# Kernel tuning notes

Hardware: AMD Instinct MI355X
Metric: run time of the kernel (lower is better)

Reference implementation:

```python
import jax, jax.numpy as jnp
import numpy as np

N, E, D_FEAT, D_HID, N_CLASS, N_LAYER = 100000, 1600000, 128, 128, 40, 2


def _sage_layer(x, x_, src, dst, wl, wr, b, n):
    # mean aggregation of neighbor (src) features into dst nodes
    agg = jax.ops.segment_sum(x[src], dst, num_segments=n)          # [N, d_in]
    cnt = jax.ops.segment_sum(jnp.ones((src.shape[0], 1), x.dtype), dst, num_segments=n)
    agg = agg / jnp.maximum(cnt, 1.0)
    h = agg @ wl + x @ wr + b        # neighbor path + root path
    h_ = x_ @ wr + b                 # twin (detached-root) stream: root weight only
    return jax.nn.relu(h), jax.nn.relu(h_)


def setup_inputs() -> dict:
    key = jax.random.key(0)
    ks = jax.random.split(key, 12)
    s = 1.0 / np.sqrt(D_HID)
    inp = {
        "x": jax.random.normal(ks[0], (N, D_FEAT), jnp.float32),
        "edge_index1": jax.random.randint(ks[1], (2, E), 0, N, jnp.int32),
        "edge_index2": jax.random.randint(ks[2], (2, E), 0, N, jnp.int32),
        "wl1": jax.random.uniform(ks[3], (D_FEAT, D_HID), jnp.float32, -s, s),
        "wr1": jax.random.uniform(ks[4], (D_FEAT, D_HID), jnp.float32, -s, s),
        "b1": jnp.zeros((D_HID,), jnp.float32),
        "wl2": jax.random.uniform(ks[5], (D_HID, D_HID), jnp.float32, -s, s),
        "wr2": jax.random.uniform(ks[6], (D_HID, D_HID), jnp.float32, -s, s),
        "b2": jnp.zeros((D_HID,), jnp.float32),
        "w_out": jax.random.uniform(ks[7], (D_HID * N_LAYER, N_CLASS), jnp.float32, -s, s),
        "b_out": jnp.zeros((N_CLASS,), jnp.float32),
        "batch_size": N,
    }
    return inp


def reference(x, edge_index1, edge_index2, wl1, wr1, b1, wl2, wr2, b2, w_out, b_out, batch_size):
    n = x.shape[0]
    x_ = jax.lax.stop_gradient(x)[:batch_size]   # detached twin stream of root nodes
    # layer 1 (dropout is eval-mode no-op)
    h1, h1_ = _sage_layer(x, x_, edge_index1[0], edge_index1[1], wl1, wr1, b1, n)
    # layer 2
    h2, h2_ = _sage_layer(h1, h1_, edge_index2[0], edge_index2[1], wl2, wr2, b2, n)
    # jumping knowledge: mode 'cat' over per-layer root representations
    h = jnp.concatenate([h1[:batch_size], h2[:batch_size]], axis=-1)
    return h @ w_out + b_out
```

## Files before the change

kernel.cpp:

```cpp
#include <hip/hip_runtime.h>


#define MAXB  512
#define CAP   24
#define CAPS  6144
#define PBLK  384

typedef __attribute__((ext_vector_type(8))) short short8;
typedef __attribute__((ext_vector_type(4))) float floatx4;

__device__ __forceinline__ unsigned short f2b(float f) {
    unsigned u = __float_as_uint(f);
    unsigned r = (u + 0x7fffu + ((u >> 16) & 1u)) >> 16;
    return (unsigned short)r;
}
__device__ __forceinline__ float lo2f(unsigned u) { return __uint_as_float(u << 16); }
__device__ __forceinline__ float hi2f(unsigned u) { return __uint_as_float(u & 0xffff0000u); }
__device__ __forceinline__ unsigned pack2(float a, float b) {
    return (unsigned)f2b(a) | ((unsigned)f2b(b) << 16);
}

__global__ __launch_bounds__(256)
void prep_hist(const float4* __restrict__ x4, uint4* __restrict__ xb4, long n8,
               const float* __restrict__ wl1, const float* __restrict__ wr1,
               const float* __restrict__ wl2, const float* __restrict__ wr2,
               const float* __restrict__ wo,
               unsigned short* __restrict__ wt1, unsigned short* __restrict__ wt2,
               unsigned short* __restrict__ wot,
               const int* __restrict__ dst1, const int* __restrict__ dst2,
               int* __restrict__ hist1, int* __restrict__ hist2,
               int* __restrict__ bptr1, int* __restrict__ bptr2,
               int* __restrict__ done, int E, int nb) {
    long i = (long)blockIdx.x * 256 + threadIdx.x;
    if (i < n8) {
        float4 a = x4[i * 2];
        float4 b = x4[i * 2 + 1];
        uint4 o;
        o.x = pack2(a.x, a.y); o.y = pack2(a.z, a.w);
        o.z = pack2(b.x, b.y); o.w = pack2(b.z, b.w);
        xb4[i] = o;
    }
    if (i < 65536) {
        int l = (int)(i >> 15);
        int k5 = (int)(i & 32767);
        int j = k5 & 7, lane = (k5 >> 3) & 63, kb = (k5 >> 9) & 7, c = k5 >> 12;
        int k = kb * 32 + (lane >> 4) * 8 + j;
        int n = c * 16 + (lane & 15);
        const float* Wl = l ? wl2 : wl1;
        const float* Wr = l ? wr2 : wr1;
        float v = (k < 128) ? Wl[k * 128 + n] : Wr[(k - 128) * 128 + n];
        (l ? wt2 : wt1)[k5] = f2b(v);
    } else if (i < 65536 + 12288) {
        int k5 = (int)(i - 65536);
        int j = k5 & 7, lane = (k5 >> 3) & 63, kb = (k5 >> 9) & 7, c = k5 >> 12;
        int k = kb * 32 + (lane >> 4) * 8 + j;
        int col = c * 16 + (lane & 15);
        float v = (col < 40) ? wo[k * 40 + col] : 0.0f;
        wot[k5] = f2b(v);
    }
    __shared__ int h[MAXB];
    __shared__ int sticket;
    if (blockIdx.x < 512) {
        const int layer = blockIdx.x >> 8;
        const int bx    = blockIdx.x & 255;
        const int* dst  = layer ? dst2 : dst1;
        int* hist       = layer ? hist2 : hist1;
        for (int k = threadIdx.x; k < nb; k += 256) h[k] = 0;
        __syncthreads();
        for (int e = bx * 256 + threadIdx.x; e < E; e += 256 * 256)
            atomicAdd(&h[dst[e] >> 8], 1);
        __syncthreads();
        for (int k = threadIdx.x; k < nb; k += 256)
            if (h[k]) atomicAdd(&hist[k], h[k]);
        __threadfence();
        if (threadIdx.x == 0) sticket = atomicAdd(done, 1);
        __syncthreads();
        if (sticket == 511) {
            int* pair = h;
            const int tt = threadIdx.x;
            for (int l = 0; l < 2; ++l) {
                int* hist = l ? hist2 : hist1;
                int* bptr = l ? bptr2 : bptr1;
                int v0 = (2 * tt < nb)     ? atomicAdd(&hist[2 * tt], 0)     : 0;
                int v1 = (2 * tt + 1 < nb) ? atomicAdd(&hist[2 * tt + 1], 0) : 0;
                pair[tt] = v0 + v1;
                __syncthreads();
                for (int off = 1; off < 256; off <<= 1) {
                    int y = (tt >= off) ? pair[tt - off] : 0;
                    __syncthreads();
                    pair[tt] += y;
                    __syncthreads();
                }
                int ebase = pair[tt] - (v0 + v1);
                if (2 * tt < nb)     bptr[2 * tt]     = ebase;
                if (2 * tt + 1 < nb) bptr[2 * tt + 1] = ebase + v0;
                if (tt == 0) bptr[nb] = E;
                __syncthreads();
            }
        }
    }
}

struct PartSmem { unsigned stage[MAXB][CAP]; int lcnt[MAXB]; int sbase[MAXB]; };
struct SortSmem { int recs[CAPS]; int sorted[CAPS]; int hcnt[256]; int hoff[256]; };
struct FusedSmem { uint4 lds[16 * 16]; };

__device__ __forceinline__ void partition_body(const int* __restrict__ src,
        const int* __restrict__ dst, const int* __restrict__ bptr,
        int* __restrict__ gcur, int* __restrict__ part, int E, int nb,
        int chunk, int nchunks, PartSmem& s) {
    const int t = threadIdx.x;
    for (int i = t; i < nb; i += 256) s.lcnt[i] = 0;
    __syncthreads();
    const int per = (E + nchunks - 1) / nchunks;
    const int e0 = chunk * per;
    const int e1 = min(e0 + per, E);
    for (int e = e0 + t; e < e1; e += 256) {
        int d = dst[e];
        int b = d >> 8;
        unsigned rec = (unsigned)src[e] | ((unsigned)(d & 255) << 17);
        int p = atomicAdd(&s.lcnt[b], 1);
        if (p < CAP) s.stage[b][p] = rec;
        else {
            int g = atomicAdd(&gcur[b], 1);
            part[bptr[b] + g] = (int)rec;
        }
    }
    __syncthreads();
    for (int b = t; b < nb; b += 256) {
        int c = s.lcnt[b]; if (c > CAP) c = CAP;
        if (c > 0) s.sbase[b] = bptr[b] + atomicAdd(&gcur[b], c);
    }
    __syncthreads();
    const int wv = t >> 6, ln = t & 63;
    for (int b = wv; b < nb; b += 4) {
        int c = s.lcnt[b]; if (c > CAP) c = CAP;
        if (ln < c) part[s.sbase[b] + ln] = (int)s.stage[b][ln];
    }
}

__device__ __forceinline__ void sort_body(const int* __restrict__ bptr,
        const int* __restrict__ part, int* __restrict__ col,
        int* __restrict__ row_ptr, int b, int nb_total, int N, int E,
        SortSmem& s) {
    const int t = threadIdx.x;
    const int beg = bptr[b], end = bptr[b + 1];
    int cnt = end - beg;
    if (cnt > CAPS) cnt = CAPS;

    for (int i = t; i < cnt; i += 256) s.recs[i] = part[beg + i];
    s.hcnt[t] = 0;
    __syncthreads();
    for (int i = t; i < cnt; i += 256)
        atomicAdd(&s.hcnt[((unsigned)s.recs[i]) >> 17], 1);
    __syncthreads();

    int v = s.hcnt[t];
    s.hoff[t] = v;
    __syncthreads();
    for (int off = 1; off < 256; off <<= 1) {
        int y = (t >= off) ? s.hoff[t - off] : 0;
        __syncthreads();
        s.hoff[t] += y;
        __syncthreads();
    }
    int myoff = s.hoff[t] - v;

    int row = b * 256 + t;
    if (row <= N) row_ptr[row] = beg + myoff;
    if (b == nb_total - 1 && t == 0) row_ptr[N] = E;
    __syncthreads();
    s.hoff[t] = myoff;
    s.hcnt[t] = 0;
    __syncthreads();

    for (int i = t; i < cnt; i += 256) {
        unsigned rec = (unsigned)s.recs[i];
        int node = rec >> 17;
        int p = s.hoff[node] + atomicAdd(&s.hcnt[node], 1);
        s.sorted[p] = (int)(rec & 0x1FFFF);
    }
    __syncthreads();
    for (int i = t; i < cnt; i += 256) col[beg + i] = s.sorted[i];
}

__device__ __forceinline__ void gather_node(const uint4* __restrict__ xb,
                                            const int* __restrict__ col,
                                            int beg, int end, int lane,
                                            float acc[8]) {
    int e = beg;
    if (e + 8 <= end) {
        int cidx[8];
#pragma unroll
        for (int q = 0; q < 8; ++q) cidx[q] = col[e + q];
        for (;;) {
            uint4 v[8];
#pragma unroll
            for (int q = 0; q < 8; ++q) v[q] = xb[(size_t)cidx[q] * 16 + lane];
            e += 8;
            const bool more = (e + 8 <= end);
            if (more) {
#pragma unroll
                for (int q = 0; q < 8; ++q) cidx[q] = col[e + q];
            }
#pragma unroll
            for (int q = 0; q < 8; ++q) {
                acc[0] += lo2f(v[q].x); acc[1] += hi2f(v[q].x);
                acc[2] += lo2f(v[q].y); acc[3] += hi2f(v[q].y);
                acc[4] += lo2f(v[q].z); acc[5] += hi2f(v[q].z);
                acc[6] += lo2f(v[q].w); acc[7] += hi2f(v[q].w);
            }
            if (!more) break;
        }
    }
    for (; e + 3 < end; e += 4) {
        uint4 v[4];
#pragma unroll
        for (int q = 0; q < 4; ++q) v[q] = xb[(size_t)col[e + q] * 16 + lane];
#pragma unroll
        for (int q = 0; q < 4; ++q) {
            acc[0] += lo2f(v[q].x); acc[1] += hi2f(v[q].x);
            acc[2] += lo2f(v[q].y); acc[3] += hi2f(v[q].y);
            acc[4] += lo2f(v[q].z); acc[5] += hi2f(v[q].z);
            acc[6] += lo2f(v[q].w); acc[7] += hi2f(v[q].w);
        }
    }
    for (; e < end; ++e) {
        uint4 v0 = xb[(size_t)col[e] * 16 + lane];
        acc[0] += lo2f(v0.x); acc[1] += hi2f(v0.x);
        acc[2] += lo2f(v0.y); acc[3] += hi2f(v0.y);
        acc[4] += lo2f(v0.z); acc[5] += hi2f(v0.z);
        acc[6] += lo2f(v0.w); acc[7] += hi2f(v0.w);
    }
    float inv = 1.0f / fmaxf((float)(end - beg), 1.0f);
#pragma unroll
    for (int j = 0; j < 8; ++j) acc[j] *= inv;
}

#define LDS_SLOT(row, col4) ((row) * 16 + ((col4) ^ ((row) & 7)))

__device__ __forceinline__ void fused1_body(const uint4* __restrict__ xb,
        const int* __restrict__ row_ptr, const int* __restrict__ col,
        const unsigned short* __restrict__ Wt, const float* __restrict__ bias,
        unsigned short* __restrict__ Hb, int N, int tile, FusedSmem& s) {
    const int t = threadIdx.x;
    {
        const int lrow = t >> 4;
        const int lane = t & 15;
        const int node = tile * 16 + lrow;
        float acc[8];
#pragma unroll
        for (int j = 0; j < 8; ++j) acc[j] = 0.0f;
        if (node < N)
            gather_node(xb, col, row_ptr[node], row_ptr[node + 1], lane, acc);
        uint4 o;
        o.x = pack2(acc[0], acc[1]); o.y = pack2(acc[2], acc[3]);
        o.z = pack2(acc[4], acc[5]); o.w = pack2(acc[6], acc[7]);
        s.lds[LDS_SLOT(lrow, lane)] = o;
    }
    __syncthreads();

    const int wave = t >> 6;
    const int lane = t & 63;
    const int quad = lane >> 4;
    const int l16  = lane & 15;
    const int rowbase = tile * 16;

    floatx4 acc2[2] = {(floatx4){0.f,0.f,0.f,0.f}, (floatx4){0.f,0.f,0.f,0.f}};
    int arow = rowbase + l16; if (arow >= N) arow = N - 1;
    const unsigned short* Xs = (const unsigned short*)xb;
    const size_t aoff = (size_t)arow * 128 + quad * 8;

#pragma unroll
    for (int kb = 0; kb < 8; ++kb) {
        short8 a;
        if (kb < 4)
            a = __builtin_bit_cast(short8, s.lds[LDS_SLOT(l16, quad + (kb & 3) * 4)]);
        else
            a = __builtin_bit_cast(short8, *(const uint4*)(Xs + aoff + (kb & 3) * 32));
#pragma unroll
        for (int cc = 0; cc < 2; ++cc) {
            const int c = wave * 2 + cc;
            short8 b = __builtin_bit_cast(short8,
                *(const uint4*)(Wt + (size_t)(((c * 8 + kb) * 64 + lane) * 8)));
            acc2[cc] = __builtin_amdgcn_mfma_f32_16x16x32_bf16(a, b, acc2[cc], 0, 0, 0);
        }
    }

#pragma unroll
    for (int cc = 0; cc < 2; ++cc) {
        const int c = wave * 2 + cc;
        const float bc = bias[c * 16 + l16];
#pragma unroll
        for (int i = 0; i < 4; ++i) {
            int row = rowbase + quad * 4 + i;
            if (row < N)
                Hb[(size_t)row * 128 + c * 16 + l16] = f2b(fmaxf(acc2[cc][i] + bc, 0.f));
        }
    }
}

__global__ __launch_bounds__(256)
void partition_l1(const int* __restrict__ ei1, const int* __restrict__ bptr1,
                  int* __restrict__ gcur1, int* __restrict__ part1, int E, int nb) {
    __shared__ PartSmem s;
    partition_body(ei1, ei1 + E, bptr1, gcur1, part1, E, nb, blockIdx.x, gridDim.x, s);
}

__global__ __launch_bounds__(256)
void sortL1_partL2(const int* __restrict__ bptr1, const int* __restrict__ part1,
                   int* __restrict__ col1, int* __restrict__ row_ptr1,
                   const int* __restrict__ ei2, const int* __restrict__ bptr2,
                   int* __restrict__ gcur2, int* __restrict__ part2,
                   int N, int E, int nb) {
    __shared__ alignas(16) char smem[sizeof(PartSmem)];
    if ((int)blockIdx.x < nb)
        sort_body(bptr1, part1, col1, row_ptr1, blockIdx.x, nb, N, E,
                  *reinterpret_cast<SortSmem*>(smem));
    else
        partition_body(ei2, ei2 + E, bptr2, gcur2, part2, E, nb,
                       blockIdx.x - nb, PBLK,
                       *reinterpret_cast<PartSmem*>(smem));
}

__global__ __launch_bounds__(256)
void sortL2_fused1(const int* __restrict__ bptr2, const int* __restrict__ part2,
                   int* __restrict__ col2, int* __restrict__ row_ptr2,
                   const uint4* __restrict__ xb, const int* __restrict__ row_ptr1,
                   const int* __restrict__ col1,
                   const unsigned short* __restrict__ wt1,
                   const float* __restrict__ b1, unsigned short* __restrict__ h1b,
                   int N, int E, int nb) {
    __shared__ alignas(16) char smem[sizeof(SortSmem)];
    if ((int)blockIdx.x < nb)
        sort_body(bptr2, part2, col2, row_ptr2, blockIdx.x, nb, N, E,
                  *reinterpret_cast<SortSmem*>(smem));
    else
        fused1_body(xb, row_ptr1, col1, wt1, b1, h1b, N, blockIdx.x - nb,
                    *reinterpret_cast<FusedSmem*>(smem));
}

__global__ __launch_bounds__(256)
void fused_layer2(const uint4* __restrict__ h1b4, const int* __restrict__ row_ptr,
                  const int* __restrict__ col,
                  const unsigned short* __restrict__ Wt,
                  const float* __restrict__ bias,
                  const unsigned short* __restrict__ Wot,
                  const float* __restrict__ bo,
                  float* __restrict__ out, int N) {
    __shared__ uint4 lds[16 * 16];
    const int t = threadIdx.x;
    {
        const int lrow = t >> 4;
        const int lane = t & 15;
        const int node = blockIdx.x * 16 + lrow;
        float acc[8];
#pragma unroll
        for (int j = 0; j < 8; ++j) acc[j] = 0.0f;
        if (node < N)
            gather_node(h1b4, col, row_ptr[node], row_ptr[node + 1], lane, acc);
        uint4 o;
        o.x = pack2(acc[0], acc[1]); o.y = pack2(acc[2], acc[3]);
        o.z = pack2(acc[4], acc[5]); o.w = pack2(acc[6], acc[7]);
        lds[LDS_SLOT(lrow, lane)] = o;
    }
    __syncthreads();

    const int wave = t >> 6;
    const int lane = t & 63;
    const int quad = lane >> 4;
    const int l16  = lane & 15;
    const int rowbase = blockIdx.x * 16;

    floatx4 acc2[2] = {(floatx4){0.f,0.f,0.f,0.f}, (floatx4){0.f,0.f,0.f,0.f}};
    floatx4 accO    = (floatx4){0.f,0.f,0.f,0.f};
    int arow = rowbase + l16; if (arow >= N) arow = N - 1;
    const unsigned short* H1s = (const unsigned short*)h1b4;
    const size_t aoff = (size_t)arow * 128 + quad * 8;

#pragma unroll
    for (int kb = 0; kb < 8; ++kb) {
        short8 a;
        if (kb < 4)
            a = __builtin_bit_cast(short8, lds[LDS_SLOT(l16, quad + (kb & 3) * 4)]);
        else
            a = __builtin_bit_cast(short8, *(const uint4*)(H1s + aoff + (kb & 3) * 32));
#pragma unroll
        for (int cc = 0; cc < 2; ++cc) {
            const int c = wave * 2 + cc;
            short8 b = __builtin_bit_cast(short8,
                *(const uint4*)(Wt + (size_t)(((c * 8 + kb) * 64 + lane) * 8)));
            acc2[cc] = __builtin_amdgcn_mfma_f32_16x16x32_bf16(a, b, acc2[cc], 0, 0, 0);
        }
        if (kb >= 4 && wave < 3) {
            short8 b = __builtin_bit_cast(short8,
                *(const uint4*)(Wot + (size_t)(((wave * 8 + (kb - 4)) * 64 + lane) * 8)));
            accO = __builtin_amdgcn_mfma_f32_16x16x32_bf16(a, b, accO, 0, 0, 0);
        }
    }

    __syncthreads();
    {
        unsigned short* lds16 = (unsigned short*)lds;
#pragma unroll
        for (int cc = 0; cc < 2; ++cc) {
            const int c = wave * 2 + cc;
            const float bc = bias[c * 16 + l16];
            const int colc = c * 16 + l16;
            const int col4 = colc >> 3;
#pragma unroll
            for (int i = 0; i < 4; ++i) {
                const int lrow = quad * 4 + i;
                lds16[LDS_SLOT(lrow, col4) * 8 + (colc & 7)] =
                    f2b(fmaxf(acc2[cc][i] + bc, 0.f));
            }
        }
    }
    __syncthreads();

    if (wave < 3) {
#pragma unroll
        for (int kh = 0; kh < 4; ++kh) {
            short8 a = __builtin_bit_cast(short8, lds[LDS_SLOT(l16, quad + kh * 4)]);
            short8 b = __builtin_bit_cast(short8,
                *(const uint4*)(Wot + (size_t)(((wave * 8 + 4 + kh) * 64 + lane) * 8)));
            accO = __builtin_amdgcn_mfma_f32_16x16x32_bf16(a, b, accO, 0, 0, 0);
        }
        const int colc = wave * 16 + l16;
        if (colc < 40) {
            const float bco = bo[colc];
#pragma unroll
            for (int i = 0; i < 4; ++i) {
                int row = rowbase + quad * 4 + i;
                if (row < N) out[(size_t)row * 40 + colc] = accO[i] + bco;
            }
        }
    }
}

extern "C" void kernel_launch(void* const* d_in, const int* in_sizes, int n_in,
                              void* d_out, int out_size, void* d_ws, size_t ws_size,
                              hipStream_t stream) {
    const float* x     = (const float*)d_in[0];
    const int*   ei1   = (const int*)d_in[1];
    const int*   ei2   = (const int*)d_in[2];
    const float* wl1   = (const float*)d_in[3];
    const float* wr1   = (const float*)d_in[4];
    const float* b1    = (const float*)d_in[5];
    const float* wl2   = (const float*)d_in[6];
    const float* wr2   = (const float*)d_in[7];
    const float* b2    = (const float*)d_in[8];
    const float* w_out = (const float*)d_in[9];
    const float* b_out = (const float*)d_in[10];

    const int N  = in_sizes[0] / 128;
    const int E  = in_sizes[1] / 2;
    const int nb = (N + 255) >> 8;

    int* hist1    = (int*)d_ws;
    int* gcur1    = hist1 + 512;
    int* hist2    = gcur1 + 512;
    int* gcur2    = hist2 + 512;
    int* bptr1    = gcur2 + 512;
    int* bptr2    = bptr1 + 513;
    int* row_ptr1 = bptr2 + 513;
    int* row_ptr2 = row_ptr1 + (N + 1);
    int* part1    = row_ptr2 + (N + 1);
    int* col1     = part1 + E;
    int* part2    = col1 + E;
    int* col2     = part2 + E;
    int* done     = gcur2 + 511;
    size_t int_cnt = (size_t)(2048 + 1026 + 2 * (N + 1)) + (size_t)4 * E;
    int_cnt = (int_cnt + 3) & ~(size_t)3;
    unsigned short* xb   = (unsigned short*)((int*)d_ws + int_cnt);
    unsigned short* h1b  = xb  + (size_t)N * 128;
    unsigned short* wt1  = h1b + (size_t)N * 128;
    unsigned short* wt2  = wt1 + 32768;
    unsigned short* wot  = wt2 + 32768;

    const long n8         = (long)N * 128 / 8;
    const int prep_blocks = (int)((n8 + 255) / 256);
    const int tile_blocks = (N + 15) / 16;

    hipMemsetAsync(hist1, 0, 2048 * sizeof(int), stream);

    prep_hist<<<prep_blocks, 256, 0, stream>>>(
        (const float4*)x, (uint4*)xb, n8, wl1, wr1, wl2, wr2, w_out,
        wt1, wt2, wot, ei1 + E, ei2 + E, hist1, hist2, bptr1, bptr2,
        done, E, nb);

    partition_l1<<<PBLK, 256, 0, stream>>>(ei1, bptr1, gcur1, part1, E, nb);

    sortL1_partL2<<<nb + PBLK, 256, 0, stream>>>(
        bptr1, part1, col1, row_ptr1, ei2, bptr2, gcur2, part2, N, E, nb);

    sortL2_fused1<<<nb + tile_blocks, 256, 0, stream>>>(
        bptr2, part2, col2, row_ptr2,
        (const uint4*)xb, row_ptr1, col1, wt1, b1, h1b, N, E, nb);

    fused_layer2<<<tile_blocks, 256, 0, stream>>>(
        (const uint4*)h1b, row_ptr2, col2, wt2, b2, wot, b_out,
        (float*)d_out, N);
}
```

Before: 431.0 us.

## Merge graph build stages into one cooperative kernel with grid syncs

Result: slower. 752.3 us (+74.6%).

```diff
diff --git a/kernel.cpp b/kernel.cpp
--- a/kernel.cpp
+++ b/kernel.cpp
@@ -1,10 +1,14 @@
 #include <hip/hip_runtime.h>
+#include <hip/hip_cooperative_groups.h>
+
+namespace cg = cooperative_groups;
 
 
 #define MAXB  512
 #define CAP   24
 #define CAPS  6144
-#define PBLK  384
+#define PCH   384
+#define HCH   384
 
 typedef __attribute__((ext_vector_type(8))) short short8;
 typedef __attribute__((ext_vector_type(4))) float floatx4;
@@ -20,90 +24,8 @@
     return (unsigned)f2b(a) | ((unsigned)f2b(b) << 16);
 }
 
-__global__ __launch_bounds__(256)
-void prep_hist(const float4* __restrict__ x4, uint4* __restrict__ xb4, long n8,
-               const float* __restrict__ wl1, const float* __restrict__ wr1,
-               const float* __restrict__ wl2, const float* __restrict__ wr2,
-               const float* __restrict__ wo,
-               unsigned short* __restrict__ wt1, unsigned short* __restrict__ wt2,
-               unsigned short* __restrict__ wot,
-               const int* __restrict__ dst1, const int* __restrict__ dst2,
-               int* __restrict__ hist1, int* __restrict__ hist2,
-               int* __restrict__ bptr1, int* __restrict__ bptr2,
-               int* __restrict__ done, int E, int nb) {
-    long i = (long)blockIdx.x * 256 + threadIdx.x;
-    if (i < n8) {
-        float4 a = x4[i * 2];
-        float4 b = x4[i * 2 + 1];
-        uint4 o;
-        o.x = pack2(a.x, a.y); o.y = pack2(a.z, a.w);
-        o.z = pack2(b.x, b.y); o.w = pack2(b.z, b.w);
-        xb4[i] = o;
-    }
-    if (i < 65536) {
-        int l = (int)(i >> 15);
-        int k5 = (int)(i & 32767);
-        int j = k5 & 7, lane = (k5 >> 3) & 63, kb = (k5 >> 9) & 7, c = k5 >> 12;
-        int k = kb * 32 + (lane >> 4) * 8 + j;
-        int n = c * 16 + (lane & 15);
-        const float* Wl = l ? wl2 : wl1;
-        const float* Wr = l ? wr2 : wr1;
-        float v = (k < 128) ? Wl[k * 128 + n] : Wr[(k - 128) * 128 + n];
-        (l ? wt2 : wt1)[k5] = f2b(v);
-    } else if (i < 65536 + 12288) {
-        int k5 = (int)(i - 65536);
-        int j = k5 & 7, lane = (k5 >> 3) & 63, kb = (k5 >> 9) & 7, c = k5 >> 12;
-        int k = kb * 32 + (lane >> 4) * 8 + j;
-        int col = c * 16 + (lane & 15);
-        float v = (col < 40) ? wo[k * 40 + col] : 0.0f;
-        wot[k5] = f2b(v);
-    }
-    __shared__ int h[MAXB];
-    __shared__ int sticket;
-    if (blockIdx.x < 512) {
-        const int layer = blockIdx.x >> 8;
-        const int bx    = blockIdx.x & 255;
-        const int* dst  = layer ? dst2 : dst1;
-        int* hist       = layer ? hist2 : hist1;
-        for (int k = threadIdx.x; k < nb; k += 256) h[k] = 0;
-        __syncthreads();
-        for (int e = bx * 256 + threadIdx.x; e < E; e += 256 * 256)
-            atomicAdd(&h[dst[e] >> 8], 1);
-        __syncthreads();
-        for (int k = threadIdx.x; k < nb; k += 256)
-            if (h[k]) atomicAdd(&hist[k], h[k]);
-        __threadfence();
-        if (threadIdx.x == 0) sticket = atomicAdd(done, 1);
-        __syncthreads();
-        if (sticket == 511) {
-            int* pair = h;
-            const int tt = threadIdx.x;
-            for (int l = 0; l < 2; ++l) {
-                int* hist = l ? hist2 : hist1;
-                int* bptr = l ? bptr2 : bptr1;
-                int v0 = (2 * tt < nb)     ? atomicAdd(&hist[2 * tt], 0)     : 0;
-                int v1 = (2 * tt + 1 < nb) ? atomicAdd(&hist[2 * tt + 1], 0) : 0;
-                pair[tt] = v0 + v1;
-                __syncthreads();
-                for (int off = 1; off < 256; off <<= 1) {
-                    int y = (tt >= off) ? pair[tt - off] : 0;
-                    __syncthreads();
-                    pair[tt] += y;
-                    __syncthreads();
-                }
-                int ebase = pair[tt] - (v0 + v1);
-                if (2 * tt < nb)     bptr[2 * tt]     = ebase;
-                if (2 * tt + 1 < nb) bptr[2 * tt + 1] = ebase + v0;
-                if (tt == 0) bptr[nb] = E;
-                __syncthreads();
-            }
-        }
-    }
-}
-
-struct PartSmem { unsigned stage[MAXB][CAP]; int lcnt[MAXB]; int sbase[MAXB]; };
+struct PartSmem { unsigned stage[MAXB][CAP]; int lcnt[MAXB]; };
 struct SortSmem { int recs[CAPS]; int sorted[CAPS]; int hcnt[256]; int hoff[256]; };
-struct FusedSmem { uint4 lds[16 * 16]; };
 
 __device__ __forceinline__ void partition_body(const int* __restrict__ src,
         const int* __restrict__ dst, const int* __restrict__ bptr,
@@ -129,13 +51,11 @@
     __syncthreads();
     for (int b = t; b < nb; b += 256) {
         int c = s.lcnt[b]; if (c > CAP) c = CAP;
-        if (c > 0) s.sbase[b] = bptr[b] + atomicAdd(&gcur[b], c);
-    }
-    __syncthreads();
-    const int wv = t >> 6, ln = t & 63;
-    for (int b = wv; b < nb; b += 4) {
-        int c = s.lcnt[b]; if (c > CAP) c = CAP;
-        if (ln < c) part[s.sbase[b] + ln] = (int)s.stage[b][ln];
+        if (c > 0) {
+            int g = atomicAdd(&gcur[b], c);
+            int base = bptr[b] + g;
+            for (int i = 0; i < c; ++i) part[base + i] = (int)s.stage[b][i];
+        }
     }
 }
 
@@ -184,6 +104,122 @@
     for (int i = t; i < cnt; i += 256) col[beg + i] = s.sorted[i];
 }
 
+struct BuildArgs {
+    const float4* x4; uint4* xb4; long n8;
+    const float* wl1; const float* wr1; const float* wl2; const float* wr2;
+    const float* wo;
+    unsigned short* wt1; unsigned short* wt2; unsigned short* wot;
+    const int* ei1; const int* ei2;
+    int* hist1; int* hist2; int* bptr1; int* bptr2;
+    int* gcur1; int* gcur2; int* part1; int* part2;
+    int* col1; int* col2; int* row_ptr1; int* row_ptr2;
+    int N; int E; int nb;
+};
+
+__global__ __launch_bounds__(256)
+void coop_build(BuildArgs a) {
+    __shared__ alignas(16) char smem[sizeof(PartSmem)];
+    cg::grid_group grid = cg::this_grid();
+    const int t = threadIdx.x;
+    const int nblk = (int)gridDim.x;
+    const long gstart = (long)blockIdx.x * 256 + t;
+    const long gstep  = (long)nblk * 256;
+
+    for (long i = gstart; i < a.n8; i += gstep) {
+        float4 va = a.x4[i * 2];
+        float4 vb = a.x4[i * 2 + 1];
+        uint4 o;
+        o.x = pack2(va.x, va.y); o.y = pack2(va.z, va.w);
+        o.z = pack2(vb.x, vb.y); o.w = pack2(vb.z, vb.w);
+        a.xb4[i] = o;
+    }
+    for (long i = gstart; i < 65536 + 12288; i += gstep) {
+        if (i < 65536) {
+            int l = (int)(i >> 15);
+            int k5 = (int)(i & 32767);
+            int j = k5 & 7, lane = (k5 >> 3) & 63, kb = (k5 >> 9) & 7, c = k5 >> 12;
+            int k = kb * 32 + (lane >> 4) * 8 + j;
+            int n = c * 16 + (lane & 15);
+            const float* Wl = l ? a.wl2 : a.wl1;
+            const float* Wr = l ? a.wr2 : a.wr1;
+            float v = (k < 128) ? Wl[k * 128 + n] : Wr[(k - 128) * 128 + n];
+            (l ? a.wt2 : a.wt1)[k5] = f2b(v);
+        } else {
+            int k5 = (int)(i - 65536);
+            int j = k5 & 7, lane = (k5 >> 3) & 63, kb = (k5 >> 9) & 7, c = k5 >> 12;
+            int k = kb * 32 + (lane >> 4) * 8 + j;
+            int col = c * 16 + (lane & 15);
+            float v = (col < 40) ? a.wo[k * 40 + col] : 0.0f;
+            a.wot[k5] = f2b(v);
+        }
+    }
+    {
+        int* h = (int*)smem;
+        for (int w = blockIdx.x; w < 2 * HCH; w += nblk) {
+            const int layer = w / HCH, bx = w % HCH;
+            const int* dst = (layer ? a.ei2 : a.ei1) + a.E;
+            int* hist      = layer ? a.hist2 : a.hist1;
+            for (int k = t; k < a.nb; k += 256) h[k] = 0;
+            __syncthreads();
+            for (int e = bx * 256 + t; e < a.E; e += HCH * 256)
+                atomicAdd(&h[dst[e] >> 8], 1);
+            __syncthreads();
+            for (int k = t; k < a.nb; k += 256)
+                if (h[k]) atomicAdd(&hist[k], h[k]);
+            __syncthreads();
+        }
+    }
+    grid.sync();
+
+    if (blockIdx.x < 2) {
+        int* pair = (int*)smem;
+        int* hist = blockIdx.x ? a.hist2 : a.hist1;
+        int* bptr = blockIdx.x ? a.bptr2 : a.bptr1;
+        int v0 = (2 * t < a.nb)     ? atomicAdd(&hist[2 * t], 0)     : 0;
+        int v1 = (2 * t + 1 < a.nb) ? atomicAdd(&hist[2 * t + 1], 0) : 0;
+        pair[t] = v0 + v1;
+        __syncthreads();
+        for (int off = 1; off < 256; off <<= 1) {
+            int y = (t >= off) ? pair[t - off] : 0;
+            __syncthreads();
+            pair[t] += y;
+            __syncthreads();
+        }
+        int ebase = pair[t] - (v0 + v1);
+        if (2 * t < a.nb)     bptr[2 * t]     = ebase;
+        if (2 * t + 1 < a.nb) bptr[2 * t + 1] = ebase + v0;
+        if (t == 0) bptr[a.nb] = a.E;
+        __threadfence();
+    }
+    grid.sync();
+
+    for (int w = blockIdx.x; w < 2 * PCH; w += nblk) {
+        const int layer = w / PCH, chunk = w % PCH;
+        const int* src = layer ? a.ei2 : a.ei1;
+        partition_body(src, src + a.E,
+                       layer ? a.bptr2 : a.bptr1,
+                       layer ? a.gcur2 : a.gcur1,
+                       layer ? a.part2 : a.part1,
+                       a.E, a.nb, chunk, PCH,
+                       *reinterpret_cast<PartSmem*>(smem));
+        __syncthreads();
+    }
+    __threadfence();
+    grid.sync();
+
+    for (int w = blockIdx.x; w < 2 * a.nb; w += nblk) {
+        const int layer = (w >= a.nb) ? 1 : 0;
+        const int b = w - layer * a.nb;
+        sort_body(layer ? a.bptr2 : a.bptr1,
+                  layer ? a.part2 : a.part1,
+                  layer ? a.col2 : a.col1,
+                  layer ? a.row_ptr2 : a.row_ptr1,
+                  b, a.nb, a.N, a.E,
+                  *reinterpret_cast<SortSmem*>(smem));
+        __syncthreads();
+    }
+}
+
 __device__ __forceinline__ void gather_node(const uint4* __restrict__ xb,
                                             const int* __restrict__ col,
                                             int beg, int end, int lane,
@@ -239,15 +275,18 @@
 
 #define LDS_SLOT(row, col4) ((row) * 16 + ((col4) ^ ((row) & 7)))
 
-__device__ __forceinline__ void fused1_body(const uint4* __restrict__ xb,
-        const int* __restrict__ row_ptr, const int* __restrict__ col,
-        const unsigned short* __restrict__ Wt, const float* __restrict__ bias,
-        unsigned short* __restrict__ Hb, int N, int tile, FusedSmem& s) {
+__global__ __launch_bounds__(256)
+void fused_layer1(const uint4* __restrict__ xb, const int* __restrict__ row_ptr,
+                  const int* __restrict__ col,
+                  const unsigned short* __restrict__ Wt,
+                  const float* __restrict__ bias,
+                  unsigned short* __restrict__ Hb, int N) {
+    __shared__ uint4 lds[16 * 16];
     const int t = threadIdx.x;
     {
         const int lrow = t >> 4;
         const int lane = t & 15;
-        const int node = tile * 16 + lrow;
+        const int node = blockIdx.x * 16 + lrow;
         float acc[8];
 #pragma unroll
         for (int j = 0; j < 8; ++j) acc[j] = 0.0f;
@@ -256,7 +295,7 @@
         uint4 o;
         o.x = pack2(acc[0], acc[1]); o.y = pack2(acc[2], acc[3]);
         o.z = pack2(acc[4], acc[5]); o.w = pack2(acc[6], acc[7]);
-        s.lds[LDS_SLOT(lrow, lane)] = o;
+        lds[LDS_SLOT(lrow, lane)] = o;
     }
     __syncthreads();
 
@@ -264,7 +303,7 @@
     const int lane = t & 63;
     const int quad = lane >> 4;
     const int l16  = lane & 15;
-    const int rowbase = tile * 16;
+    const int rowbase = blockIdx.x * 16;
 
     floatx4 acc2[2] = {(floatx4){0.f,0.f,0.f,0.f}, (floatx4){0.f,0.f,0.f,0.f}};
     int arow = rowbase + l16; if (arow >= N) arow = N - 1;
@@ -275,7 +314,7 @@
     for (int kb = 0; kb < 8; ++kb) {
         short8 a;
         if (kb < 4)
-            a = __builtin_bit_cast(short8, s.lds[LDS_SLOT(l16, quad + (kb & 3) * 4)]);
+            a = __builtin_bit_cast(short8, lds[LDS_SLOT(l16, quad + (kb & 3) * 4)]);
         else
             a = __builtin_bit_cast(short8, *(const uint4*)(Xs + aoff + (kb & 3) * 32));
 #pragma unroll
@@ -298,46 +337,6 @@
                 Hb[(size_t)row * 128 + c * 16 + l16] = f2b(fmaxf(acc2[cc][i] + bc, 0.f));
         }
     }
-}
-
-__global__ __launch_bounds__(256)
-void partition_l1(const int* __restrict__ ei1, const int* __restrict__ bptr1,
-                  int* __restrict__ gcur1, int* __restrict__ part1, int E, int nb) {
-    __shared__ PartSmem s;
-    partition_body(ei1, ei1 + E, bptr1, gcur1, part1, E, nb, blockIdx.x, gridDim.x, s);
-}
-
-__global__ __launch_bounds__(256)
-void sortL1_partL2(const int* __restrict__ bptr1, const int* __restrict__ part1,
-                   int* __restrict__ col1, int* __restrict__ row_ptr1,
-                   const int* __restrict__ ei2, const int* __restrict__ bptr2,
-                   int* __restrict__ gcur2, int* __restrict__ part2,
-                   int N, int E, int nb) {
-    __shared__ alignas(16) char smem[sizeof(PartSmem)];
-    if ((int)blockIdx.x < nb)
-        sort_body(bptr1, part1, col1, row_ptr1, blockIdx.x, nb, N, E,
-                  *reinterpret_cast<SortSmem*>(smem));
-    else
-        partition_body(ei2, ei2 + E, bptr2, gcur2, part2, E, nb,
-                       blockIdx.x - nb, PBLK,
-                       *reinterpret_cast<PartSmem*>(smem));
-}
-
-__global__ __launch_bounds__(256)
-void sortL2_fused1(const int* __restrict__ bptr2, const int* __restrict__ part2,
-                   int* __restrict__ col2, int* __restrict__ row_ptr2,
-                   const uint4* __restrict__ xb, const int* __restrict__ row_ptr1,
-                   const int* __restrict__ col1,
-                   const unsigned short* __restrict__ wt1,
-                   const float* __restrict__ b1, unsigned short* __restrict__ h1b,
-                   int N, int E, int nb) {
-    __shared__ alignas(16) char smem[sizeof(SortSmem)];
-    if ((int)blockIdx.x < nb)
-        sort_body(bptr2, part2, col2, row_ptr2, blockIdx.x, nb, N, E,
-                  *reinterpret_cast<SortSmem*>(smem));
-    else
-        fused1_body(xb, row_ptr1, col1, wt1, b1, h1b, N, blockIdx.x - nb,
-                    *reinterpret_cast<FusedSmem*>(smem));
 }
 
 __global__ __launch_bounds__(256)
@@ -469,7 +468,6 @@
     int* col1     = part1 + E;
     int* part2    = col1 + E;
     int* col2     = part2 + E;
-    int* done     = gcur2 + 511;
     size_t int_cnt = (size_t)(2048 + 1026 + 2 * (N + 1)) + (size_t)4 * E;
     int_cnt = (int_cnt + 3) & ~(size_t)3;
     unsigned short* xb   = (unsigned short*)((int*)d_ws + int_cnt);
@@ -479,25 +477,39 @@
     unsigned short* wot  = wt2 + 32768;
 
     const long n8         = (long)N * 128 / 8;
-    const int prep_blocks = (int)((n8 + 255) / 256);
     const int tile_blocks = (N + 15) / 16;
 
+    static int coop_grid = 0;
+    if (coop_grid == 0) {
+        int occ = 0;
+        hipOccupancyMaxActiveBlocksPerMultiprocessor(
+            &occ, (const void*)coop_build, 256, 0);
+        int dev = 0, cus = 0;
+        hipGetDevice(&dev);
+        hipDeviceGetAttribute(&cus, hipDeviceAttributeMultiprocessorCount, dev);
+        long cap = (long)occ * (long)cus;
+        coop_grid = (int)(cap < 768 ? cap : 768);
+        if (coop_grid < 2) coop_grid = 2;
+    }
+
     hipMemsetAsync(hist1, 0, 2048 * sizeof(int), stream);
 
-    prep_hist<<<prep_blocks, 256, 0, stream>>>(
-        (const float4*)x, (uint4*)xb, n8, wl1, wr1, wl2, wr2, w_out,
-        wt1, wt2, wot, ei1 + E, ei2 + E, hist1, hist2, bptr1, bptr2,
-        done, E, nb);
-
-    partition_l1<<<PBLK, 256, 0, stream>>>(ei1, bptr1, gcur1, part1, E, nb);
-
-    sortL1_partL2<<<nb + PBLK, 256, 0, stream>>>(
-        bptr1, part1, col1, row_ptr1, ei2, bptr2, gcur2, part2, N, E, nb);
-
-    sortL2_fused1<<<nb + tile_blocks, 256, 0, stream>>>(
-        bptr2, part2, col2, row_ptr2,
-        (const uint4*)xb, row_ptr1, col1, wt1, b1, h1b, N, E, nb);
-
+    BuildArgs ba;
+    ba.x4 = (const float4*)x; ba.xb4 = (uint4*)xb; ba.n8 = n8;
+    ba.wl1 = wl1; ba.wr1 = wr1; ba.wl2 = wl2; ba.wr2 = wr2; ba.wo = w_out;
+    ba.wt1 = wt1; ba.wt2 = wt2; ba.wot = wot;
+    ba.ei1 = ei1; ba.ei2 = ei2;
+    ba.hist1 = hist1; ba.hist2 = hist2; ba.bptr1 = bptr1; ba.bptr2 = bptr2;
+    ba.gcur1 = gcur1; ba.gcur2 = gcur2; ba.part1 = part1; ba.part2 = part2;
+    ba.col1 = col1; ba.col2 = col2; ba.row_ptr1 = row_ptr1; ba.row_ptr2 = row_ptr2;
+    ba.N = N; ba.E = E; ba.nb = nb;
+
+    void* params[] = { &ba };
+    hipLaunchCooperativeKernel((const void*)coop_build, dim3(coop_grid),
+                               dim3(256), params, 0, stream);
+
+    fused_layer1<<<tile_blocks, 256, 0, stream>>>(
+        (const uint4*)xb, row_ptr1, col1, wt1, b1, h1b, N);
     fused_layer2<<<tile_blocks, 256, 0, stream>>>(
         (const uint4*)h1b, row_ptr2, col2, wt2, b2, wot, b_out,
         (float*)d_out, N);
```
